# Optimization experiments

Hardware: AMD Instinct MI355X
Metric: run time of the kernel (lower is better)

Reference implementation:

```python
import jax, jax.numpy as jnp
import numpy as np

B, N, T, CIN, HID, EMB, K = 32, 256, 13, 2, 64, 10, 2


def setup_inputs() -> dict:
    key = jax.random.key(0)
    ks = jax.random.split(key, 24)
    r = lambda i, shape, s=1.0: jax.random.normal(ks[i], shape, jnp.float32) * s
    return {
        "times": jnp.arange(T, dtype=jnp.float32),
        # natural cubic spline coefficients: (B, N, T-1, CIN)
        "coeff_a": r(0, (B, N, T - 1, CIN)),
        "coeff_b": r(1, (B, N, T - 1, CIN), 0.1),
        "coeff_two_c": r(2, (B, N, T - 1, CIN), 0.1),
        "coeff_three_d": r(3, (B, N, T - 1, CIN), 0.1),
        # initial_h / initial_z linear layers (input -> hidden)
        "W_h": r(4, (CIN, HID), 0.5), "b_h": r(5, (HID,), 0.1),
        "W_z": r(6, (CIN, HID), 0.5), "b_z": r(7, (HID,), 0.1),
        # func_f (FinalTanh_f): linear_in, one hidden linear, linear_out -> hidden*input
        "Wf_in": r(8, (HID, HID), 0.1), "bf_in": r(9, (HID,), 0.05),
        "Wf_hid": r(10, (HID, HID), 0.1), "bf_hid": r(11, (HID,), 0.05),
        "Wf_out": r(12, (HID, HID * CIN), 0.1), "bf_out": r(13, (HID * CIN,), 0.05),
        # func_g (VectorField_g, g_type='agc')
        "Wg_in": r(14, (HID, HID), 0.1), "bg_in": r(15, (HID,), 0.05),
        "Eg": r(16, (N, EMB)),
        "W_pool": r(17, (EMB, K, HID, HID), 0.1),
        "b_pool": r(18, (EMB, HID), 0.1),
        "Wg_out": r(19, (HID, HID * CIN), 0.1), "bg_out": r(20, (HID * CIN,), 0.05),
    }


def reference(times, coeff_a, coeff_b, coeff_two_c, coeff_three_d,
              W_h, b_h, W_z, b_z,
              Wf_in, bf_in, Wf_hid, bf_hid, Wf_out, bf_out,
              Wg_in, bg_in, Eg, W_pool, b_pool, Wg_out, bg_out):
    maxidx = coeff_b.shape[-2] - 1

    def dX_dt(t):  # NaturalCubicSpline.derivative
        idx = jnp.clip(jnp.searchsorted(times, t, side='right') - 1, 0, maxidx)
        frac = t - times[idx]
        b = coeff_b[..., idx, :]
        c = coeff_two_c[..., idx, :]
        d = coeff_three_d[..., idx, :]
        return b + (c + d * frac) * frac  # (B, N, CIN)

    # adaptive graph conv (agc) static pieces, cheb_k = 2
    A = jax.nn.softmax(jax.nn.relu(Eg @ Eg.T), axis=1)          # (N, N)
    supports = jnp.stack([jnp.eye(N, dtype=A.dtype), A])        # (K, N, N)
    Wn = jnp.einsum('nd,dkio->nkio', Eg, W_pool)                # (N, K, HID, HID)
    bn = Eg @ b_pool                                            # (N, HID)

    def func_f(h):  # FinalTanh_f: MLP -> (B, N, HID, CIN) field
        x = jax.nn.relu(h @ Wf_in + bf_in)
        x = jax.nn.relu(x @ Wf_hid + bf_hid)
        x = (x @ Wf_out + bf_out).reshape(*x.shape[:-1], HID, CIN)
        return jnp.tanh(x)

    def func_g(z):  # VectorField_g with agc
        x = jax.nn.relu(z @ Wg_in + bg_in)                       # (B, N, HID)
        x_g = jnp.einsum('knm,bmc->bnkc', supports, x)           # (B, N, K, HID)
        x = jnp.einsum('bnki,nkio->bno', x_g, Wn) + bn           # (B, N, HID)
        x = (x @ Wg_out + bg_out).reshape(*x.shape[:-1], HID, CIN)
        return jnp.tanh(x)

    def vf(t, h, z):  # VectorField_g_dev of cdeint_gde_dev
        dX = dX_dt(t)                                            # (B, N, CIN)
        f = func_f(h)
        g = func_g(z)
        dh = jnp.einsum('bnhi,bni->bnh', f, dX)
        dz = jnp.einsum('bnhi,bni->bnh', g * f, dX)
        return dh, dz

    # spline.evaluate(times[0]) == coeff_a[..., 0, :] (frac = 0)
    x0 = coeff_a[..., 0, :]
    h0 = x0 @ W_h + b_h
    z0 = x0 @ W_z + b_z

    third = jnp.float32(1.0 / 3.0)

    def step(carry, ts):  # torchdiffeq 'rk4' (3/8 rule), one step per interval
        h, z = carry
        t0, t1 = ts
        dt = t1 - t0
        k1h, k1z = vf(t0, h, z)
        k2h, k2z = vf(t0 + dt * third, h + dt * third * k1h, z + dt * third * k1z)
        k3h, k3z = vf(t0 + dt * 2 * third, h + dt * (k2h - third * k1h), z + dt * (k2z - third * k1z))
        k4h, k4z = vf(t1, h + dt * (k1h - k2h + k3h), z + dt * (k1z - k2z + k3z))
        h = h + dt * 0.125 * (k1h + 3.0 * (k2h + k3h) + k4h)
        z = z + dt * 0.125 * (k1z + 3.0 * (k2z + k3z) + k4z)
        return (h, z), z

    ts = jnp.stack([times[:-1], times[1:]], axis=1)              # (T-1, 2)
    (_, _), z_seq = jax.lax.scan(step, (h0, z0), ts)
    z_t = jnp.concatenate([z0[None], z_seq], axis=0)             # (T, B, N, HID)
    return jnp.transpose(z_t, (1, 2, 0, 3))                      # (B, N, T, HID)
```

## Files before the change

kernel.cpp:

```cpp
#include <hip/hip_runtime.h>

typedef unsigned short ushort_t;
typedef unsigned int uint_t;

#define CW_OFF  0
#define A_OFF   524288
#define BN_OFF  786432
#define WN_OFF  851968
#define XB_OFF  5046272
#define H_OFF   7143424
#define Z_OFF   9240576
#define K1H_OFF 11337728
#define K1Z_OFF 13434880
#define K2H_OFF 15532032
#define K2Z_OFF 17629184
#define UH_OFF  19726336

#define F_X0     0
#define F_WH     16384
#define F_BH     16512
#define F_WZ     16576
#define F_BZ     16704
#define F_WFIN   16768
#define F_BFIN   20864
#define F_WFHID  20928
#define F_BFHID  25024
#define F_WFOUT  25088
#define F_BFOUT  33280
#define F_WGIN   33408
#define F_BGIN   37504
#define F_WGOUT  37568
#define F_BGOUT  45760
#define F_EG     45888
#define F_WPOOL  48448
#define F_BPOOL  130368

__device__ __forceinline__ float bfl(uint_t u){ union{uint_t i; float f;} c; c.i = u<<16; return c.f; }
__device__ __forceinline__ float bfh(uint_t u){ union{uint_t i; float f;} c; c.i = u & 0xffff0000u; return c.f; }
__device__ __forceinline__ float bf1(ushort_t u){ union{uint_t i; float f;} c; c.i = ((uint_t)u)<<16; return c.f; }
__device__ __forceinline__ uint_t f2bf(float x){
  uint_t u = __float_as_uint(x);
  uint_t r = u + 0x7fffu + ((u >> 16) & 1u);
  return r >> 16;
}
__device__ __forceinline__ float fast_tanh(float x){
  float e = __expf(2.0f*x);
  return 1.0f - 2.0f/(e+1.0f);
}
__device__ __forceinline__ bool inputs_are_f32(const void* times){
  return ((const uint_t*)times)[0] != 0x3F800000u;
}

__device__ __forceinline__ void dotf_4(const float* act, const float* W, int o0, float acc[4]) {
  const float4* a4 = (const float4*)act;
  #pragma unroll
  for (int i4 = 0; i4 < 16; ++i4) {
    float4 av4 = a4[i4];
    float av[4] = {av4.x, av4.y, av4.z, av4.w};
    #pragma unroll
    for (int ii = 0; ii < 4; ++ii) {
      float4 w = *(const float4*)(W + (i4*4+ii)*64 + o0);
      acc[0] += av[ii]*w.x; acc[1] += av[ii]*w.y;
      acc[2] += av[ii]*w.z; acc[3] += av[ii]*w.w;
    }
  }
}

__device__ __forceinline__ void dotf_8(const float* act, const float* W, int co0, float acc[8]) {
  const float4* a4 = (const float4*)act;
  #pragma unroll
  for (int i4 = 0; i4 < 16; ++i4) {
    float4 av4 = a4[i4];
    float av[4] = {av4.x, av4.y, av4.z, av4.w};
    #pragma unroll
    for (int ii = 0; ii < 4; ++ii) {
      const float* wp = W + (i4*4+ii)*128 + co0;
      float4 w0 = *(const float4*)(wp);
      float4 w1 = *(const float4*)(wp + 4);
      float a = av[ii];
      acc[0] += a*w0.x; acc[1] += a*w0.y; acc[2] += a*w0.z; acc[3] += a*w0.w;
      acc[4] += a*w1.x; acc[5] += a*w1.y; acc[6] += a*w1.z; acc[7] += a*w1.w;
    }
  }
}

__global__ __launch_bounds__(256) void k_conv(
    const void* times, const void* ca,
    const void* W_h, const void* b_h, const void* W_z, const void* b_z,
    const void* Wf_in, const void* bf_in, const void* Wf_hid, const void* bf_hid,
    const void* Wf_out, const void* bf_out, const void* Wg_in, const void* bg_in,
    const void* Wg_out, const void* bg_out, const void* Eg, const void* W_pool,
    const void* b_pool, char* __restrict__ wsb)
{
  const bool f32in = inputs_are_f32(times);
  float* F = (float*)(wsb + CW_OFF);
  if (blockIdx.x == 0) {
    for (int i = threadIdx.x; i < 16384; i += 256) {
      int si = (i >> 1)*24 + (i & 1);
      F[F_X0 + i] = f32in ? ((const float*)ca)[si] : bf1(((const ushort_t*)ca)[si]);
    }
    return;
  }
  const void* src = nullptr; int dst = 0, cnt = 0;
  switch (blockIdx.x) {
    case 1:  src = W_h;    dst = F_WH;    cnt = 128;   break;
    case 2:  src = b_h;    dst = F_BH;    cnt = 64;    break;
    case 3:  src = W_z;    dst = F_WZ;    cnt = 128;   break;
    case 4:  src = b_z;    dst = F_BZ;    cnt = 64;    break;
    case 5:  src = Wf_in;  dst = F_WFIN;  cnt = 4096;  break;
    case 6:  src = bf_in;  dst = F_BFIN;  cnt = 64;    break;
    case 7:  src = Wf_hid; dst = F_WFHID; cnt = 4096;  break;
    case 8:  src = bf_hid; dst = F_BFHID; cnt = 64;    break;
    case 9:  src = Wf_out; dst = F_WFOUT; cnt = 8192;  break;
    case 10: src = bf_out; dst = F_BFOUT; cnt = 128;   break;
    case 11: src = Wg_in;  dst = F_WGIN;  cnt = 4096;  break;
    case 12: src = bg_in;  dst = F_BGIN;  cnt = 64;    break;
    case 13: src = Wg_out; dst = F_WGOUT; cnt = 8192;  break;
    case 14: src = bg_out; dst = F_BGOUT; cnt = 128;   break;
    case 15: src = Eg;     dst = F_EG;    cnt = 2560;  break;
    case 16: src = W_pool; dst = F_WPOOL; cnt = 81920; break;
    default: src = b_pool; dst = F_BPOOL; cnt = 640;   break;
  }
  for (int i = threadIdx.x; i < cnt; i += 256)
    F[dst + i] = f32in ? ((const float*)src)[i] : bf1(((const ushort_t*)src)[i]);
}

__global__ __launch_bounds__(256) void k_A(char* __restrict__ wsb) {
  const float* F = (const float*)(wsb + CW_OFF);
  float* Aw = (float*)(wsb + A_OFF);
  float* bn = (float*)(wsb + BN_OFF);
  const int nrow = blockIdx.x;
  const int m = threadIdx.x;
  float eg_n[10];
  #pragma unroll
  for (int d = 0; d < 10; ++d) eg_n[d] = F[F_EG + nrow*10 + d];
  float dot = 0.f;
  #pragma unroll
  for (int d = 0; d < 10; ++d) dot += eg_n[d] * F[F_EG + m*10 + d];
  float v = fmaxf(dot, 0.f);
  __shared__ float red[256];
  red[m] = v; __syncthreads();
  for (int off = 128; off > 0; off >>= 1) {
    if (m < off) red[m] = fmaxf(red[m], red[m+off]);
    __syncthreads();
  }
  float vmax = red[0]; __syncthreads();
  float e = __expf(v - vmax);
  red[m] = e; __syncthreads();
  for (int off = 128; off > 0; off >>= 1) {
    if (m < off) red[m] += red[m+off];
    __syncthreads();
  }
  float ssum = red[0];
  Aw[nrow*256 + m] = e / ssum;
  if (m < 64) {
    float acc = 0.f;
    #pragma unroll
    for (int d = 0; d < 10; ++d) acc += eg_n[d] * F[F_BPOOL + d*64 + m];
    bn[nrow*64 + m] = acc;
  }
}

__global__ __launch_bounds__(256) void k_Wn(char* __restrict__ wsb) {
  const float* F = (const float*)(wsb + CW_OFF);
  ushort_t* Wn = (ushort_t*)(wsb + WN_OFF);
  int idx = blockIdx.x*256 + threadIdx.x;
  int o = idx & 63;
  int i = (idx >> 6) & 63;
  int k = (idx >> 12) & 1;
  int n = idx >> 13;
  float acc = 0.f;
  #pragma unroll
  for (int d = 0; d < 10; ++d)
    acc += F[F_EG + n*10 + d] * F[F_WPOOL + ((d*2 + k)*64 + i)*64 + o];
  Wn[idx] = (ushort_t)f2bf(acc);
}

__global__ __launch_bounds__(512) void k_init2(char* __restrict__ wsb, float* __restrict__ out) {
  const float* F = (const float*)(wsb + CW_OFF);
  float* H = (float*)(wsb + H_OFF);
  float* Z = (float*)(wsb + Z_OFF);
  ushort_t* X0 = (ushort_t*)(wsb + XB_OFF);

  const int tid = threadIdx.x;
  const int lr  = tid >> 4;
  const int o0  = (tid & 15) * 4;
  const int row = blockIdx.x * 32 + lr;

  __shared__ __align__(16) float sIn[32][68];

  float a0 = F[F_X0 + row*2 + 0];
  float a1 = F[F_X0 + row*2 + 1];
  float h[4], z[4];
  #pragma unroll
  for (int j = 0; j < 4; ++j) {
    h[j] = a0*F[F_WH + o0+j] + a1*F[F_WH + 64+o0+j] + F[F_BH + o0+j];
    z[j] = a0*F[F_WZ + o0+j] + a1*F[F_WZ + 64+o0+j] + F[F_BZ + o0+j];
  }
  *(float4*)(H + row*64 + o0) = make_float4(h[0],h[1],h[2],h[3]);
  *(float4*)(Z + row*64 + o0) = make_float4(z[0],z[1],z[2],z[3]);
  *(float4*)(out + (row*13)*64 + o0) = make_float4(z[0],z[1],z[2],z[3]);

  *(float4*)&sIn[lr][o0] = make_float4(z[0],z[1],z[2],z[3]);
  __syncthreads();
  float xr[4];
  { float4 bv = *(const float4*)(F + F_BGIN + o0);
    xr[0]=bv.x; xr[1]=bv.y; xr[2]=bv.z; xr[3]=bv.w; }
  dotf_4(&sIn[lr][0], F + F_WGIN, o0, xr);
  #pragma unroll
  for (int j=0;j<4;++j) xr[j] = fmaxf(xr[j], 0.f);
  { uint2 pk;
    pk.x = f2bf(xr[0]) | (f2bf(xr[1]) << 16);
    pk.y = f2bf(xr[2]) | (f2bf(xr[3]) << 16);
    *(uint2*)(X0 + row*64 + o0) = pk; }
}

__global__ __launch_bounds__(512) void k_stage(
    const void* __restrict__ times,
    const void* __restrict__ cbv, const void* __restrict__ ccv, const void* __restrict__ cdv,
    char* __restrict__ wsb, float* __restrict__ out, int vfc)
{
  const float* F  = (const float*)(wsb + CW_OFF);
  const float* Aw = (const float*)(wsb + A_OFF);
  const float* bn = (const float*)(wsb + BN_OFF);
  const ushort_t* Wn = (const ushort_t*)(wsb + WN_OFF);
  ushort_t* XB = (ushort_t*)(wsb + XB_OFF);
  float* H   = (float*)(wsb + H_OFF);
  float* Z   = (float*)(wsb + Z_OFF);
  float* K1h = (float*)(wsb + K1H_OFF);
  float* K1z = (float*)(wsb + K1Z_OFF);
  float* K2h = (float*)(wsb + K2H_OFF);
  float* K2z = (float*)(wsb + K2Z_OFF);
  float* UH  = (float*)(wsb + UH_OFF);
  const bool f32in = inputs_are_f32(times);

  const int s  = vfc >> 2;
  const int st = vfc & 3;
  const ushort_t* Xc = XB + (vfc & 1) * 524288;
  ushort_t*       Xn = XB + ((vfc + 1) & 1) * 524288;

  const int tid = threadIdx.x;
  const int lr  = tid >> 4;
  const int t16 = tid & 15;
  const int o0  = t16 * 4;
  const int co0 = o0 * 2;
  const int bb  = blockIdx.x >> 3;
  const int nr  = blockIdx.x & 7;
  const int n   = nr * 32 + lr;
  const int row = bb * 256 + n;

  __shared__ __align__(16) float sIn[32][68];
  __shared__ __align__(16) float sT [32][68];
  __shared__ __align__(16) float sX [32][68];
  __shared__ __align__(16) float xs [128][68];

  { uint2 w = *(const uint2*)(Xc + row*64 + o0);
    *(float4*)&sX[lr][o0] = make_float4(bfl(w.x), bfh(w.x), bfl(w.y), bfh(w.y)); }

  float y[4] = {0.f,0.f,0.f,0.f};
  const float* Arow = Aw + n*256;
  #pragma unroll 1
  for (int half = 0; half < 2; ++half) {
    __syncthreads();
    #pragma unroll
    for (int q = tid; q < 2048; q += 512) {
      int r = q >> 4, c4 = q & 15;
      uint2 w = *(const uint2*)(Xc + (bb*256 + half*128 + r)*64 + c4*4);
      *(float4*)&xs[r][c4*4] = make_float4(bfl(w.x), bfh(w.x), bfl(w.y), bfh(w.y));
    }
    __syncthreads();
    #pragma unroll 4
    for (int m4 = 0; m4 < 32; ++m4) {
      float4 av = *(const float4*)(Arow + half*128 + m4*4);
      float am[4] = {av.x, av.y, av.z, av.w};
      #pragma unroll
      for (int mm = 0; mm < 4; ++mm) {
        float4 xv = *(const float4*)&xs[m4*4+mm][o0];
        y[0] += am[mm]*xv.x; y[1] += am[mm]*xv.y;
        y[2] += am[mm]*xv.z; y[3] += am[mm]*xv.w;
      }
    }
  }

  __syncthreads();
  *(float4*)&sT[lr][o0] = make_float4(y[0],y[1],y[2],y[3]);
  __syncthreads();
  float og[4];
  { float4 bv = *(const float4*)(bn + n*64 + o0); og[0]=bv.x; og[1]=bv.y; og[2]=bv.z; og[3]=bv.w; }
  const ushort_t* W0 = Wn + n*8192;
  #pragma unroll
  for (int i4 = 0; i4 < 16; ++i4) {
    float4 xa = *(const float4*)&sX[lr][i4*4];
    float4 ya = *(const float4*)&sT[lr][i4*4];
    float xav[4]={xa.x,xa.y,xa.z,xa.w};
    float yav[4]={ya.x,ya.y,ya.z,ya.w};
    #pragma unroll
    for (int ii = 0; ii < 4; ++ii) {
      int i = i4*4 + ii;
      uint2 w0 = *(const uint2*)(W0 + i*64 + o0);
      uint2 w1 = *(const uint2*)(W0 + 4096 + i*64 + o0);
      og[0] += xav[ii]*bfl(w0.x) + yav[ii]*bfl(w1.x);
      og[1] += xav[ii]*bfh(w0.x) + yav[ii]*bfh(w1.x);
      og[2] += xav[ii]*bfl(w0.y) + yav[ii]*bfl(w1.y);
      og[3] += xav[ii]*bfh(w0.y) + yav[ii]*bfh(w1.y);
    }
  }
  *(float4*)&sIn[lr][o0] = make_float4(og[0],og[1],og[2],og[3]);
  __syncthreads();
  float go[8];
  { float4 b0 = *(const float4*)(F + F_BGOUT + co0);
    float4 b1 = *(const float4*)(F + F_BGOUT + co0 + 4);
    go[0]=b0.x; go[1]=b0.y; go[2]=b0.z; go[3]=b0.w;
    go[4]=b1.x; go[5]=b1.y; go[6]=b1.z; go[7]=b1.w; }
  dotf_8(&sIn[lr][0], F + F_WGOUT, co0, go);
  float g0[4], g1[4];
  #pragma unroll
  for (int j=0;j<4;++j){ g0[j]=fast_tanh(go[2*j]); g1[j]=fast_tanh(go[2*j+1]); }

  __syncthreads();
  { const float* UHsrc = (st == 0) ? H : UH;
    float4 uv = *(const float4*)(UHsrc + row*64 + o0);
    *(float4*)&sIn[lr][o0] = uv; }
  __syncthreads();
  float a1v[4];
  { float4 bv = *(const float4*)(F + F_BFIN + o0);
    a1v[0]=bv.x; a1v[1]=bv.y; a1v[2]=bv.z; a1v[3]=bv.w; }
  dotf_4(&sIn[lr][0], F + F_WFIN, o0, a1v);
  #pragma unroll
  for (int j=0;j<4;++j) a1v[j] = fmaxf(a1v[j], 0.f);
  *(float4*)&sT[lr][o0] = make_float4(a1v[0],a1v[1],a1v[2],a1v[3]);
  __syncthreads();
  float a2v[4];
  { float4 bv = *(const float4*)(F + F_BFHID + o0);
    a2v[0]=bv.x; a2v[1]=bv.y; a2v[2]=bv.z; a2v[3]=bv.w; }
  dotf_4(&sT[lr][0], F + F_WFHID, o0, a2v);
  #pragma unroll
  for (int j=0;j<4;++j) a2v[j] = fmaxf(a2v[j], 0.f);
  *(float4*)&sIn[lr][o0] = make_float4(a2v[0],a2v[1],a2v[2],a2v[3]);
  __syncthreads();
  float fo[8];
  { float4 b0 = *(const float4*)(F + F_BFOUT + co0);
    float4 b1 = *(const float4*)(F + F_BFOUT + co0 + 4);
    fo[0]=b0.x; fo[1]=b0.y; fo[2]=b0.z; fo[3]=b0.w;
    fo[4]=b1.x; fo[5]=b1.y; fo[6]=b1.z; fo[7]=b1.w; }
  dotf_8(&sIn[lr][0], F + F_WFOUT, co0, fo);
  float f0[4], f1[4];
  #pragma unroll
  for (int j=0;j<4;++j){ f0[j]=fast_tanh(fo[2*j]); f1[j]=fast_tanh(fo[2*j+1]); }

  int sidx; float frac;
  if (st == 0)      { sidx = s; frac = 0.f; }
  else if (st == 1) { sidx = s; frac = 0.33333334f; }
  else if (st == 2) { sidx = s; frac = 0.66666669f; }
  else              { sidx = (s < 11) ? s+1 : 11; frac = (s < 11) ? 0.f : 1.f; }
  float dX0, dX1;
  if (f32in) {
    float2 vb = *(const float2*)((const float*)cbv + (row*12 + sidx)*2);
    float2 vc = *(const float2*)((const float*)ccv + (row*12 + sidx)*2);
    float2 vd = *(const float2*)((const float*)cdv + (row*12 + sidx)*2);
    dX0 = vb.x + (vc.x + vd.x*frac)*frac;
    dX1 = vb.y + (vc.y + vd.y*frac)*frac;
  } else {
    uint_t vb = *(const uint_t*)((const ushort_t*)cbv + (row*12 + sidx)*2);
    uint_t vc = *(const uint_t*)((const ushort_t*)ccv + (row*12 + sidx)*2);
    uint_t vd = *(const uint_t*)((const ushort_t*)cdv + (row*12 + sidx)*2);
    dX0 = bfl(vb) + (bfl(vc) + bfl(vd)*frac)*frac;
    dX1 = bfh(vb) + (bfh(vc) + bfh(vd)*frac)*frac;
  }

  float dh[4], dz[4];
  #pragma unroll
  for (int j=0;j<4;++j){
    dh[j] = f0[j]*dX0 + f1[j]*dX1;
    dz[j] = g0[j]*f0[j]*dX0 + g1[j]*f1[j]*dX1;
  }

  float uh_n[4], uz_n[4];
  float4 hv = *(const float4*)(H + row*64 + o0);
  float4 zv = *(const float4*)(Z + row*64 + o0);
  float h[4] = {hv.x,hv.y,hv.z,hv.w};
  float z[4] = {zv.x,zv.y,zv.z,zv.w};

  if (st == 0) {
    *(float4*)(K1h + row*64 + o0) = make_float4(dh[0],dh[1],dh[2],dh[3]);
    *(float4*)(K1z + row*64 + o0) = make_float4(dz[0],dz[1],dz[2],dz[3]);
    #pragma unroll
    for (int j=0;j<4;++j){ uh_n[j]=h[j]+dh[j]*(1.f/3.f); uz_n[j]=z[j]+dz[j]*(1.f/3.f); }
  } else if (st == 1) {
    float4 k1hv = *(const float4*)(K1h + row*64 + o0);
    float4 k1zv = *(const float4*)(K1z + row*64 + o0);
    float k1hl[4]={k1hv.x,k1hv.y,k1hv.z,k1hv.w};
    float k1zl[4]={k1zv.x,k1zv.y,k1zv.z,k1zv.w};
    float Qh[4],Qz[4],Ph[4],Pz[4];
    #pragma unroll
    for (int j=0;j<4;++j){
      Qh[j]=k1hl[j]+3.f*dh[j]; Qz[j]=k1zl[j]+3.f*dz[j];
      Ph[j]=k1hl[j]-dh[j];     Pz[j]=k1zl[j]-dz[j];
      uh_n[j]=h[j]+dh[j]-k1hl[j]*(1.f/3.f);
      uz_n[j]=z[j]+dz[j]-k1zl[j]*(1.f/3.f);
    }
    *(float4*)(K1h + row*64 + o0) = make_float4(Qh[0],Qh[1],Qh[2],Qh[3]);
    *(float4*)(K1z + row*64 + o0) = make_float4(Qz[0],Qz[1],Qz[2],Qz[3]);
    *(float4*)(K2h + row*64 + o0) = make_float4(Ph[0],Ph[1],Ph[2],Ph[3]);
    *(float4*)(K2z + row*64 + o0) = make_float4(Pz[0],Pz[1],Pz[2],Pz[3]);
  } else if (st == 2) {
    float4 Qhv = *(const float4*)(K1h + row*64 + o0);
    float4 Qzv = *(const float4*)(K1z + row*64 + o0);
    float4 Phv = *(const float4*)(K2h + row*64 + o0);
    float4 Pzv = *(const float4*)(K2z + row*64 + o0);
    float Qh[4]={Qhv.x,Qhv.y,Qhv.z,Qhv.w}, Qz[4]={Qzv.x,Qzv.y,Qzv.z,Qzv.w};
    float Ph[4]={Phv.x,Phv.y,Phv.z,Phv.w}, Pz[4]={Pzv.x,Pzv.y,Pzv.z,Pzv.w};
    float Ah[4],Az[4];
    #pragma unroll
    for (int j=0;j<4;++j){
      Ah[j]=Qh[j]+3.f*dh[j]; Az[j]=Qz[j]+3.f*dz[j];
      uh_n[j]=h[j]+Ph[j]+dh[j];
      uz_n[j]=z[j]+Pz[j]+dz[j];
    }
    *(float4*)(K1h + row*64 + o0) = make_float4(Ah[0],Ah[1],Ah[2],Ah[3]);
    *(float4*)(K1z + row*64 + o0) = make_float4(Az[0],Az[1],Az[2],Az[3]);
  } else {
    float4 Ahv = *(const float4*)(K1h + row*64 + o0);
    float4 Azv = *(const float4*)(K1z + row*64 + o0);
    #pragma unroll
    for (int j=0;j<4;++j){
      float hn = h[j] + 0.125f*(((const float*)&Ahv)[j] + dh[j]);
      float zn = z[j] + 0.125f*(((const float*)&Azv)[j] + dz[j]);
      uh_n[j]=hn; uz_n[j]=zn;
    }
    *(float4*)(H + row*64 + o0) = make_float4(uh_n[0],uh_n[1],uh_n[2],uh_n[3]);
    *(float4*)(Z + row*64 + o0) = make_float4(uz_n[0],uz_n[1],uz_n[2],uz_n[3]);
    *(float4*)(out + (row*13 + s + 1)*64 + o0) = make_float4(uz_n[0],uz_n[1],uz_n[2],uz_n[3]);
  }

  if (vfc < 47) {
    *(float4*)(UH + row*64 + o0) = make_float4(uh_n[0],uh_n[1],uh_n[2],uh_n[3]);
    __syncthreads();
    *(float4*)&sIn[lr][o0] = make_float4(uz_n[0],uz_n[1],uz_n[2],uz_n[3]);
    __syncthreads();
    float xr[4];
    { float4 bv = *(const float4*)(F + F_BGIN + o0);
      xr[0]=bv.x; xr[1]=bv.y; xr[2]=bv.z; xr[3]=bv.w; }
    dotf_4(&sIn[lr][0], F + F_WGIN, o0, xr);
    #pragma unroll
    for (int j=0;j<4;++j) xr[j] = fmaxf(xr[j], 0.f);
    uint2 pk;
    pk.x = f2bf(xr[0]) | (f2bf(xr[1]) << 16);
    pk.y = f2bf(xr[2]) | (f2bf(xr[3]) << 16);
    *(uint2*)(Xn + row*64 + o0) = pk;
  }
}

extern "C" void kernel_launch(void* const* d_in, const int* in_sizes, int n_in,
                              void* d_out, int out_size, void* d_ws, size_t ws_size,
                              hipStream_t stream) {
  const void* times   = d_in[0];
  const void* coeff_a = d_in[1];
  const void* coeff_b = d_in[2];
  const void* coeff_c = d_in[3];
  const void* coeff_d = d_in[4];
  const void* W_h    = d_in[5];
  const void* b_h    = d_in[6];
  const void* W_z    = d_in[7];
  const void* b_z    = d_in[8];
  const void* Wf_in  = d_in[9];
  const void* bf_in  = d_in[10];
  const void* Wf_hid = d_in[11];
  const void* bf_hid = d_in[12];
  const void* Wf_out = d_in[13];
  const void* bf_out = d_in[14];
  const void* Wg_in  = d_in[15];
  const void* bg_in  = d_in[16];
  const void* Eg     = d_in[17];
  const void* W_pool = d_in[18];
  const void* b_pool = d_in[19];
  const void* Wg_out = d_in[20];
  const void* bg_out = d_in[21];

  char* wsb = (char*)d_ws;
  float* out = (float*)d_out;

  hipLaunchKernelGGL(k_conv, dim3(18), dim3(256), 0, stream,
                     times, coeff_a, W_h, b_h, W_z, b_z,
                     Wf_in, bf_in, Wf_hid, bf_hid, Wf_out, bf_out,
                     Wg_in, bg_in, Wg_out, bg_out, Eg, W_pool, b_pool, wsb);
  hipLaunchKernelGGL(k_A,  dim3(256),  dim3(256), 0, stream, wsb);
  hipLaunchKernelGGL(k_Wn, dim3(8192), dim3(256), 0, stream, wsb);
  hipLaunchKernelGGL(k_init2, dim3(256), dim3(512), 0, stream, wsb, out);
  for (int vfc = 0; vfc < 48; ++vfc) {
    hipLaunchKernelGGL(k_stage, dim3(256), dim3(512), 0, stream,
                       times, coeff_b, coeff_c, coeff_d, wsb, out, vfc);
  }
}
```

Measured before the change: 5.064 ms.

## Split stage into graph-conv kernel and node-major kernel with shared-memory Wn

Splits each vector-field stage kernel in two. The first computes the A·X graph convolution and writes Y as bf16. The second assigns one block per node across all 32 batches, so that node's 16 KB bf16 Wn slice is loaded once into LDS as fp32 and reused by every batch row. Previously each block re-read per-node Wn from global memory for every row. The cost is twice as many launches (96 stage launches), an extra Y round trip through global memory, and about 35 KB more LDS per block, which may lower occupancy.

```diff
diff --git a/kernel.cpp b/kernel.cpp
--- a/kernel.cpp
+++ b/kernel.cpp
@@ -7,7 +7,8 @@
 #define A_OFF   524288
 #define BN_OFF  786432
 #define WN_OFF  851968
-#define XB_OFF  5046272
+#define X_OFF   5046272
+#define Y_OFF   6094848
 #define H_OFF   7143424
 #define Z_OFF   9240576
 #define K1H_OFF 11337728
@@ -180,7 +181,7 @@
   const float* F = (const float*)(wsb + CW_OFF);
   float* H = (float*)(wsb + H_OFF);
   float* Z = (float*)(wsb + Z_OFF);
-  ushort_t* X0 = (ushort_t*)(wsb + XB_OFF);
+  ushort_t* X0 = (ushort_t*)(wsb + X_OFF);
 
   const int tid = threadIdx.x;
   const int lr  = tid >> 4;
@@ -215,47 +216,20 @@
     *(uint2*)(X0 + row*64 + o0) = pk; }
 }
 
-__global__ __launch_bounds__(512) void k_stage(
-    const void* __restrict__ times,
-    const void* __restrict__ cbv, const void* __restrict__ ccv, const void* __restrict__ cdv,
-    char* __restrict__ wsb, float* __restrict__ out, int vfc)
-{
-  const float* F  = (const float*)(wsb + CW_OFF);
+__global__ __launch_bounds__(512) void k_conv_y(char* __restrict__ wsb) {
   const float* Aw = (const float*)(wsb + A_OFF);
-  const float* bn = (const float*)(wsb + BN_OFF);
-  const ushort_t* Wn = (const ushort_t*)(wsb + WN_OFF);
-  ushort_t* XB = (ushort_t*)(wsb + XB_OFF);
-  float* H   = (float*)(wsb + H_OFF);
-  float* Z   = (float*)(wsb + Z_OFF);
-  float* K1h = (float*)(wsb + K1H_OFF);
-  float* K1z = (float*)(wsb + K1Z_OFF);
-  float* K2h = (float*)(wsb + K2H_OFF);
-  float* K2z = (float*)(wsb + K2Z_OFF);
-  float* UH  = (float*)(wsb + UH_OFF);
-  const bool f32in = inputs_are_f32(times);
-
-  const int s  = vfc >> 2;
-  const int st = vfc & 3;
-  const ushort_t* Xc = XB + (vfc & 1) * 524288;
-  ushort_t*       Xn = XB + ((vfc + 1) & 1) * 524288;
+  const ushort_t* Xg = (const ushort_t*)(wsb + X_OFF);
+  ushort_t* Yg = (ushort_t*)(wsb + Y_OFF);
 
   const int tid = threadIdx.x;
   const int lr  = tid >> 4;
-  const int t16 = tid & 15;
-  const int o0  = t16 * 4;
-  const int co0 = o0 * 2;
+  const int o0  = (tid & 15) * 4;
   const int bb  = blockIdx.x >> 3;
   const int nr  = blockIdx.x & 7;
   const int n   = nr * 32 + lr;
   const int row = bb * 256 + n;
 
-  __shared__ __align__(16) float sIn[32][68];
-  __shared__ __align__(16) float sT [32][68];
-  __shared__ __align__(16) float sX [32][68];
-  __shared__ __align__(16) float xs [128][68];
-
-  { uint2 w = *(const uint2*)(Xc + row*64 + o0);
-    *(float4*)&sX[lr][o0] = make_float4(bfl(w.x), bfh(w.x), bfl(w.y), bfh(w.y)); }
+  __shared__ __align__(16) float xs[128][68];
 
   float y[4] = {0.f,0.f,0.f,0.f};
   const float* Arow = Aw + n*256;
@@ -265,7 +239,7 @@
     #pragma unroll
     for (int q = tid; q < 2048; q += 512) {
       int r = q >> 4, c4 = q & 15;
-      uint2 w = *(const uint2*)(Xc + (bb*256 + half*128 + r)*64 + c4*4);
+      uint2 w = *(const uint2*)(Xg + (bb*256 + half*128 + r)*64 + c4*4);
       *(float4*)&xs[r][c4*4] = make_float4(bfl(w.x), bfh(w.x), bfl(w.y), bfh(w.y));
     }
     __syncthreads();
@@ -281,13 +255,62 @@
       }
     }
   }
-
-  __syncthreads();
-  *(float4*)&sT[lr][o0] = make_float4(y[0],y[1],y[2],y[3]);
-  __syncthreads();
+  uint2 pk;
+  pk.x = f2bf(y[0]) | (f2bf(y[1]) << 16);
+  pk.y = f2bf(y[2]) | (f2bf(y[3]) << 16);
+  *(uint2*)(Yg + row*64 + o0) = pk;
+}
+
+__global__ __launch_bounds__(512) void k_og(
+    const void* __restrict__ times,
+    const void* __restrict__ cbv, const void* __restrict__ ccv, const void* __restrict__ cdv,
+    char* __restrict__ wsb, float* __restrict__ out, int vfc)
+{
+  const float* F  = (const float*)(wsb + CW_OFF);
+  const float* bn = (const float*)(wsb + BN_OFF);
+  const ushort_t* Wn = (const ushort_t*)(wsb + WN_OFF);
+  ushort_t* Xg = (ushort_t*)(wsb + X_OFF);
+  const ushort_t* Yg = (const ushort_t*)(wsb + Y_OFF);
+  float* H   = (float*)(wsb + H_OFF);
+  float* Z   = (float*)(wsb + Z_OFF);
+  float* K1h = (float*)(wsb + K1H_OFF);
+  float* K1z = (float*)(wsb + K1Z_OFF);
+  float* K2h = (float*)(wsb + K2H_OFF);
+  float* K2z = (float*)(wsb + K2Z_OFF);
+  float* UH  = (float*)(wsb + UH_OFF);
+  const bool f32in = inputs_are_f32(times);
+
+  const int s  = vfc >> 2;
+  const int st = vfc & 3;
+
+  const int tid = threadIdx.x;
+  const int lr  = tid >> 4;
+  const int t16 = tid & 15;
+  const int o0  = t16 * 4;
+  const int co0 = o0 * 2;
+  const int n   = blockIdx.x;
+  const int row = lr * 256 + n;
+
+  __shared__ __align__(16) float sIn[32][68];
+  __shared__ __align__(16) float sT [32][68];
+  __shared__ __align__(16) float sX [32][68];
+  __shared__ __align__(16) float wn [2][64][68];
+
+  { const ushort_t* Wsrc = Wn + n*8192;
+    #pragma unroll
+    for (int e = tid*4; e < 8192; e += 2048) {
+      uint2 w = *(const uint2*)(Wsrc + e);
+      int k = e >> 12, i = (e >> 6) & 63, o = e & 63;
+      *(float4*)&wn[k][i][o] = make_float4(bfl(w.x), bfh(w.x), bfl(w.y), bfh(w.y));
+    } }
+  { uint2 w = *(const uint2*)(Xg + row*64 + o0);
+    *(float4*)&sX[lr][o0] = make_float4(bfl(w.x), bfh(w.x), bfl(w.y), bfh(w.y)); }
+  { uint2 w = *(const uint2*)(Yg + row*64 + o0);
+    *(float4*)&sT[lr][o0] = make_float4(bfl(w.x), bfh(w.x), bfl(w.y), bfh(w.y)); }
+  __syncthreads();
+
   float og[4];
   { float4 bv = *(const float4*)(bn + n*64 + o0); og[0]=bv.x; og[1]=bv.y; og[2]=bv.z; og[3]=bv.w; }
-  const ushort_t* W0 = Wn + n*8192;
   #pragma unroll
   for (int i4 = 0; i4 < 16; ++i4) {
     float4 xa = *(const float4*)&sX[lr][i4*4];
@@ -297,14 +320,15 @@
     #pragma unroll
     for (int ii = 0; ii < 4; ++ii) {
       int i = i4*4 + ii;
-      uint2 w0 = *(const uint2*)(W0 + i*64 + o0);
-      uint2 w1 = *(const uint2*)(W0 + 4096 + i*64 + o0);
-      og[0] += xav[ii]*bfl(w0.x) + yav[ii]*bfl(w1.x);
-      og[1] += xav[ii]*bfh(w0.x) + yav[ii]*bfh(w1.x);
-      og[2] += xav[ii]*bfl(w0.y) + yav[ii]*bfl(w1.y);
-      og[3] += xav[ii]*bfh(w0.y) + yav[ii]*bfh(w1.y);
-    }
-  }
+      float4 w0 = *(const float4*)&wn[0][i][o0];
+      float4 w1 = *(const float4*)&wn[1][i][o0];
+      og[0] += xav[ii]*w0.x + yav[ii]*w1.x;
+      og[1] += xav[ii]*w0.y + yav[ii]*w1.y;
+      og[2] += xav[ii]*w0.z + yav[ii]*w1.z;
+      og[3] += xav[ii]*w0.w + yav[ii]*w1.w;
+    }
+  }
+  __syncthreads();
   *(float4*)&sIn[lr][o0] = make_float4(og[0],og[1],og[2],og[3]);
   __syncthreads();
   float go[8];
@@ -447,7 +471,7 @@
     uint2 pk;
     pk.x = f2bf(xr[0]) | (f2bf(xr[1]) << 16);
     pk.y = f2bf(xr[2]) | (f2bf(xr[3]) << 16);
-    *(uint2*)(Xn + row*64 + o0) = pk;
+    *(uint2*)(Xg + row*64 + o0) = pk;
   }
 }
 
@@ -488,7 +512,8 @@
   hipLaunchKernelGGL(k_Wn, dim3(8192), dim3(256), 0, stream, wsb);
   hipLaunchKernelGGL(k_init2, dim3(256), dim3(512), 0, stream, wsb, out);
   for (int vfc = 0; vfc < 48; ++vfc) {
-    hipLaunchKernelGGL(k_stage, dim3(256), dim3(512), 0, stream,
+    hipLaunchKernelGGL(k_conv_y, dim3(256), dim3(512), 0, stream, wsb);
+    hipLaunchKernelGGL(k_og, dim3(256), dim3(512), 0, stream,
                        times, coeff_b, coeff_c, coeff_d, wsb, out, vfc);
   }
 }
```

After: 5.286 ms. 4.4% more time.
